# Optimization experiments

Measured on AMD Instinct MI355X. Metric: run time of the kernel, lower is better.

## Reference

```python
import jax, jax.numpy as jnp
import numpy as np

N = 30          # num_nodes
F = 4           # feature_dim
H = 64          # decoder_hidden_dim
TF = 2          # decoder_tf_interval
MIN_VAR = 1e-8
MAX_VAR = 100.0

_pairs = np.array([(i, j) for i in range(N) for j in range(N) if i != j])
RECV = jnp.asarray(_pairs[:, 0])   # [E] receiver node per edge
SEND = jnp.asarray(_pairs[:, 1])   # [E] sender node per edge


def _mlp(x, Ws, bs, softplus=False):
    # Linear->ReLU for all hidden layers, final Linear; optional softplus+clip head
    for W, b in zip(Ws[:-1], bs[:-1]):
        x = jax.nn.relu(x @ W + b)
    x = x @ Ws[-1] + bs[-1]
    if softplus:
        x = jnp.clip(jax.nn.softplus(x), MIN_VAR, MAX_VAR)
    return x


def setup_inputs() -> dict:
    key = jax.random.key(0)
    ks = jax.random.split(key, 20)
    B, S, T = 8, 4, 128
    E = N * (N - 1)

    def lin(k, din, dout):
        s = 1.0 / np.sqrt(din)
        return jax.random.uniform(k, (din, dout), jnp.float32, -s, s)

    inp = {
        'data': jax.random.normal(ks[0], (B, S, T, N, F), jnp.float32),
        'graph': (jax.random.uniform(ks[1], (B * S, E)) > 0.5).astype(jnp.float32),
        # msg_fc: 2F -> H -> H
        'msg_W1': lin(ks[2], 2 * F, H), 'msg_b1': jnp.zeros((H,), jnp.float32),
        'msg_W2': lin(ks[3], H, H),     'msg_b2': jnp.zeros((H,), jnp.float32),
        # mean_fc: H -> H -> H -> F
        'mean_W1': lin(ks[4], H, H), 'mean_b1': jnp.zeros((H,), jnp.float32),
        'mean_W2': lin(ks[5], H, H), 'mean_b2': jnp.zeros((H,), jnp.float32),
        'mean_W3': lin(ks[6], H, F), 'mean_b3': jnp.zeros((F,), jnp.float32),
        # variance_fc: H -> H -> H -> F (softplus + clip)
        'var_W1': lin(ks[7], H, H), 'var_b1': jnp.zeros((H,), jnp.float32),
        'var_W2': lin(ks[8], H, H), 'var_b2': jnp.zeros((H,), jnp.float32),
        'var_W3': lin(ks[9], H, F), 'var_b3': jnp.zeros((F,), jnp.float32),
    }
    return inp


def _single_step(prev, graph, p):
    # prev: [B, C, N, F]; graph: [B, E]
    edge_hidden = jnp.concatenate([prev[:, :, RECV, :], prev[:, :, SEND, :]], axis=-1)  # [B,C,E,2F]
    msg = _mlp(edge_hidden, [p['msg_W1'], p['msg_W2']], [p['msg_b1'], p['msg_b2']])     # [B,C,E,H]
    msg = msg * graph[:, None, :, None]
    B, C = prev.shape[0], prev.shape[1]
    # edge2node: sum messages into receiver nodes (normalize=False)
    agg = jnp.zeros((B, C, N, msg.shape[-1]), msg.dtype).at[:, :, RECV, :].add(msg)     # [B,C,N,H]
    mu = _mlp(agg, [p['mean_W1'], p['mean_W2'], p['mean_W3']],
              [p['mean_b1'], p['mean_b2'], p['mean_b3']])
    var = _mlp(agg, [p['var_W1'], p['var_W2'], p['var_W3']],
               [p['var_b1'], p['var_b2'], p['var_b3']], softplus=True)
    return mu, var


def reference(data, graph, msg_W1, msg_b1, msg_W2, msg_b2,
              mean_W1, mean_b1, mean_W2, mean_b2, mean_W3, mean_b3,
              var_W1, var_b1, var_W2, var_b2, var_W3, var_b3):
    p = dict(msg_W1=msg_W1, msg_b1=msg_b1, msg_W2=msg_W2, msg_b2=msg_b2,
             mean_W1=mean_W1, mean_b1=mean_b1, mean_W2=mean_W2, mean_b2=mean_b2,
             mean_W3=mean_W3, mean_b3=mean_b3,
             var_W1=var_W1, var_b1=var_b1, var_W2=var_W2, var_b2=var_b2,
             var_W3=var_W3, var_b3=var_b3)
    B, S, T, Nn, Ff = data.shape
    x = data.reshape(B * S, T, Nn, Ff)
    prev = x[:, ::TF]                       # teacher-forced anchors, [B*S, C, N, F]
    C = prev.shape[1]
    mus, vars = [], []
    for _ in range(TF):
        mu, var = _single_step(prev, graph, p)
        mus.append(mu)
        vars.append(var)
        prev = mu
    # interleave: out[:, i::TF] = step_i
    mu_pred = jnp.stack(mus, axis=2).reshape(B * S, C * TF, Nn, Ff)[:, :T - 1]
    var_pred = jnp.stack(vars, axis=2).reshape(B * S, C * TF, Nn, Ff)[:, :T - 1]
    mu_pred = mu_pred.reshape(B, S, T - 1, Nn, Ff)
    var_pred = var_pred.reshape(B, S, T - 1, Nn, Ff)
    return mu_pred, var_pred
```

## Files before the change

kernel.cpp:

```cpp
#include <hip/hip_runtime.h>
#include <hip/hip_bf16.h>
#include <hip/hip_fp16.h>

typedef unsigned short u16;
typedef unsigned int u32;
typedef __attribute__((ext_vector_type(4))) short short4v;
typedef __attribute__((ext_vector_type(4))) float f32x4;
typedef __attribute__((ext_vector_type(2))) _Float16 half2v;

#define NN 30
#define FF 4
#define EE 870
#define BSZ 32
#define CC 64
#define TT 128
#define NF 120
#define TSTRIDE 15240
#define OUTHALF 487680
#define AST 68
#define WST 68
#define NSETS 4
#define BPB  16

#define WS_WOFF 256
#define WS_MASKOFF (256 + 45056)

__device__ __forceinline__ float bf2f(u16 u) {
    union { u32 i; float f; } v; v.i = ((u32)u) << 16; return v.f;
}
__device__ __forceinline__ u16 f2bf(float f) {
    __hip_bfloat16 h = __float2bfloat16(f); return *(u16*)&h;
}
__device__ __forceinline__ u16 f2bf_fast(float f) {
    union { float f; u32 u; } v; v.f = f;
    return (u16)((v.u + 0x7FFFu + ((v.u >> 16) & 1u)) >> 16);
}
__device__ __forceinline__ float ldv(const void* p, int idx, int isbf) {
    if (isbf) return bf2f(((const u16*)p)[idx]);
    return ((const float*)p)[idx];
}
__device__ __forceinline__ float softplus_clip(float z) {
    float t = __expf(-fabsf(z));
    float sp = fmaxf(z, 0.f) + __logf(1.f + t);
    return fminf(fmaxf(sp, 1e-8f), 100.f);
}
__device__ __forceinline__ f32x4 MFMA16(short4v a, short4v b, f32x4 c) {
    return __builtin_amdgcn_mfma_f32_16x16x16bf16_1k(a, b, c, 0, 0, 0);
}

__device__ __forceinline__ int probe_isbf(const u16* g, int lane) {
    int hit = (g[2 * lane] == 0x3F80u) | (g[128 + 2 * lane] == 0x3F80u);
    unsigned long long b = __ballot(hit);
    return (b != 0ull) ? 1 : 0;
}

__global__ void prep_ws(const void* __restrict__ mW2,
                        const void* __restrict__ aW1, const void* __restrict__ aW2,
                        const void* __restrict__ vW1, const void* __restrict__ vW2,
                        const void* __restrict__ graph,
                        u16* __restrict__ wsW, u32* __restrict__ wsMask) {
    const int lane = threadIdx.x & 63;
    const int isbf = probe_isbf((const u16*)graph, lane);
    const int gtid = blockIdx.x * blockDim.x + threadIdx.x;
    const int gstr = gridDim.x * blockDim.x;
    for (int idx = gtid; idx < 4096; idx += gstr) {
        int k = idx >> 6, o = idx & 63;
        int d = o * 64 + k;
        wsW[d]         = f2bf(ldv(mW2, idx, isbf));
        wsW[4096 + d]  = f2bf(ldv(aW1, idx, isbf));
        wsW[8192 + d]  = f2bf(ldv(aW2, idx, isbf));
        wsW[12288 + d] = f2bf(ldv(vW1, idx, isbf));
        wsW[16384 + d] = f2bf(ldv(vW2, idx, isbf));
    }
    for (int idx = gtid; idx < BSZ * NN; idx += gstr) {
        int b = idx / NN, i = idx % NN;
        u32 m = 0;
        for (int e = 0; e < 29; e++)
            if (ldv(graph, b * EE + i * 29 + e, isbf) > 0.5f) m |= (1u << e);
        wsMask[idx] = m;
    }
}

__global__ __launch_bounds__(1024, 4)
void sim_fused(const void* __restrict__ data,
               const void* __restrict__ graph,
               const void* __restrict__ mW1, const void* __restrict__ mB1,
               const void* __restrict__ mB2,
               const void* __restrict__ aB1, const void* __restrict__ aB2,
               const void* __restrict__ aB3,
               const void* __restrict__ vB1, const void* __restrict__ vB2,
               const void* __restrict__ vB3,
               const void* __restrict__ aW3, const void* __restrict__ vW3,
               const u16* __restrict__ wsW, const u32* __restrict__ wsMask,
               void* __restrict__ out)
{
    __shared__ __align__(16) float xN[NSETS][NF];
    __shared__ __align__(16) u32 gmaskS[32];
    __shared__ __align__(16) u16 S[NSETS][32 * AST];
    __shared__ __align__(16) u16 lwM2[64 * WST];
    __shared__ __align__(16) u16 lwH1m[64 * WST];
    __shared__ __align__(16) u16 lwH2m[64 * WST];
    __shared__ __align__(16) u16 lwH1v[64 * WST];
    __shared__ __align__(16) u16 lwH2v[64 * WST];
    __shared__ __align__(16) float biasL[5 * 64];

    const int tid  = threadIdx.x;
    const int lane = tid & 63;
    const int wv   = tid >> 6;
    const int set  = wv >> 2;
    const int swv  = wv & 3;
    const int ln15 = lane & 15;
    const int quad = lane >> 4;
    const int bs   = blockIdx.x / BPB;
    const int bg   = blockIdx.x % BPB;
    const int c    = bg * NSETS + set;
    const int isbf = probe_isbf((const u16*)graph, lane);

    const bool isMean = (swv < 2);
    const int nb = swv & 1;

    {
        const u32* w32 = (const u32*)wsW;
        for (int idx = tid; idx < 2048; idx += 1024) {
            int o = idx >> 5, kw = idx & 31;
            int d = o * (WST / 2) + kw;
            ((u32*)lwM2)[d]  = w32[idx];
            ((u32*)lwH1m)[d] = w32[2048 + idx];
            ((u32*)lwH2m)[d] = w32[4096 + idx];
            ((u32*)lwH1v)[d] = w32[6144 + idx];
            ((u32*)lwH2v)[d] = w32[8192 + idx];
        }
    }
    if (tid < 64) {
        biasL[tid]       = ldv(mB2, tid, isbf);
        biasL[64 + tid]  = ldv(aB1, tid, isbf);
        biasL[128 + tid] = ldv(aB2, tid, isbf);
        biasL[192 + tid] = ldv(vB1, tid, isbf);
        biasL[256 + tid] = ldv(vB2, tid, isbf);
    }
    if (tid < 32) gmaskS[tid] = (tid < NN) ? wsMask[bs * NN + tid] : 0u;
    if (tid < 512) {
        int s2 = tid >> 7, row = 30 + ((tid >> 6) & 1);
        S[s2][row * AST + (tid & 63)] = 0;
    }

    float w1r[8];
#pragma unroll
    for (int k = 0; k < 8; k++) w1r[k] = ldv(mW1, k * 64 + lane, isbf);
    const float b1r = ldv(mB1, lane, isbf);
    float b3r[4];
#pragma unroll
    for (int r = 0; r < 4; r++) b3r[r] = ldv(isMean ? aB3 : vB3, r, isbf);

    const u16* wH1 = isMean ? lwH1m : lwH1v;
    const u16* wH2 = isMean ? lwH2m : lwH2v;
    const float* bAgg = biasL;
    const float* bH1  = isMean ? (biasL + 64)  : (biasL + 192);
    const float* bH2  = isMean ? (biasL + 128) : (biasL + 256);

    const void* W3src = isMean ? aW3 : vW3;
    short4v eA[4];
#pragma unroll
    for (int kb = 0; kb < 4; kb++) {
        union { short4v v; u16 s[4]; } pk;
#pragma unroll
        for (int j = 0; j < 4; j++) {
            int k = kb * 16 + quad * 4 + j;
            pk.s[j] = (ln15 < 4)
                ? (isbf ? ((const u16*)W3src)[k * 4 + ln15]
                        : f2bf(((const float*)W3src)[k * 4 + ln15]))
                : (u16)0;
        }
        eA[kb] = pk.v;
    }

    __syncthreads();

    const int myNode = nb * 16 + ln15;
    const float ngp = (myNode < NN) ? (float)__popc(gmaskS[myNode]) : 0.f;

    auto runLayer = [&](const u16* wl, const float* bl, const short4v* Bin,
                        short4v* Bout, float bscale, bool doRelu) {
#pragma unroll
        for (int fb = 0; fb < 4; fb++) {
            f32x4 acc = {0.f, 0.f, 0.f, 0.f};
#pragma unroll
            for (int kb = 0; kb < 4; kb++) {
                short4v a = *(const short4v*)&wl[(fb * 16 + ln15) * WST + kb * 16 + quad * 4];
                acc = MFMA16(a, Bin[kb], acc);
            }
            float4 bv = *(const float4*)&bl[fb * 16 + quad * 4];
            union { short4v v; u16 s[4]; } pk;
#pragma unroll
            for (int r = 0; r < 4; r++) {
                float val = acc[r] + bscale * (&bv.x)[r];
                if (doRelu) val = fmaxf(val, 0.f);
                pk.s[r] = f2bf_fast(val);
            }
            Bout[fb] = pk.v;
        }
    };

    const int setTid = tid & 255;

    if (isbf) {
        if (setTid < 60) {
            u32 w = ((const u32*)data)[((bs * TT + 2 * c) * NF) / 2 + setTid];
            xN[set][setTid * 2]     = bf2f((u16)(w & 0xFFFF));
            xN[set][setTid * 2 + 1] = bf2f((u16)(w >> 16));
        }
    } else {
        if (setTid < NF) xN[set][setTid] = ((const float*)data)[(bs * TT + 2 * c) * NF + setTid];
    }
    __syncthreads();

    for (int step = 0; step < 2; step++) {
        half2v pJp[15];
#pragma unroll
        for (int m = 0; m < 15; m++) {
            float4 xa = *(const float4*)&xN[set][(2 * m) * 4];
            float4 xb = *(const float4*)&xN[set][(2 * m + 1) * 4];
            float pa = xa.x * w1r[4] + xa.y * w1r[5] + xa.z * w1r[6] + xa.w * w1r[7];
            float pb = xb.x * w1r[4] + xb.y * w1r[5] + xb.z * w1r[6] + xb.w * w1r[7];
            half2v p; p.x = (_Float16)pa; p.y = (_Float16)pb;
            pJp[m] = p;
        }

        const half2v zero2 = {(_Float16)0.f, (_Float16)0.f};
        for (int i = swv; i < NN; i += 4) {
            float4 xv = *(const float4*)&xN[set][i * 4];
            float pI = b1r + xv.x * w1r[0] + xv.y * w1r[1] + xv.z * w1r[2] + xv.w * w1r[3];
            _Float16 pih = (_Float16)pI;
            half2v pIp = {pih, pih};
            u32 gm = gmaskS[i];
            u32 lowm = (1u << i) - 1u;
            u32 m2 = __builtin_amdgcn_readfirstlane((gm & lowm) | ((gm & ~lowm) << 1));
            float s0 = 0.f, s1 = 0.f;
#pragma unroll
            for (int m = 0; m < 15; m++) {
                half2v t = pIp + pJp[m];
                t = __builtin_elementwise_max(t, zero2);
#if __has_builtin(__builtin_amdgcn_fdot2)
                u32 mm = ((m2 >> (2 * m)) & 1u) * 0x3C00u
                       + ((m2 >> (2 * m + 1)) & 1u) * 0x3C000000u;
                half2v mv = __builtin_bit_cast(half2v, mm);
                if (m & 1) s1 = __builtin_amdgcn_fdot2(t, mv, s1, false);
                else       s0 = __builtin_amdgcn_fdot2(t, mv, s0, false);
#else
                u32 mb = ((m2 >> (2 * m)) & 1u) * 0xFFFFu
                       + ((m2 >> (2 * m + 1)) & 1u) * 0xFFFF0000u;
                u32 tb = __builtin_bit_cast(u32, t) & mb;
                half2v tv = __builtin_bit_cast(half2v, tb);
                s0 += (float)tv.x; s1 += (float)tv.y;
#endif
            }
            S[set][i * AST + lane] = f2bf_fast(s0 + s1);
        }
        __syncthreads();

        short4v Bs[4], Ba[4], Bb[4];
#pragma unroll
        for (int kb = 0; kb < 4; kb++)
            Bs[kb] = *(const short4v*)&S[set][(nb * 16 + ln15) * AST + kb * 16 + quad * 4];

        runLayer(lwM2, bAgg, Bs, Ba, ngp, false);
        runLayer(wH1,  bH1,  Ba, Bb, 1.f, true);
        runLayer(wH2,  bH2,  Bb, Ba, 1.f, true);

        {
            f32x4 acc = {0.f, 0.f, 0.f, 0.f};
#pragma unroll
            for (int kb = 0; kb < 4; kb++) acc = MFMA16(eA[kb], Ba[kb], acc);
            const int n = nb * 16 + ln15;
            const int t = 2 * c + step;
            if (quad == 0 && n < NN) {
                float v[4];
#pragma unroll
                for (int r = 0; r < 4; r++) v[r] = acc[r] + b3r[r];
                if (!isMean) {
#pragma unroll
                    for (int r = 0; r < 4; r++) v[r] = softplus_clip(v[r]);
                }
                if (t < 127) {
                    size_t o = (size_t)bs * TSTRIDE + (size_t)t * NF + n * 4
                             + (isMean ? 0 : OUTHALF);
                    if (isbf) {
                        u16* op = (u16*)out;
                        u32 lo = (u32)f2bf_fast(v[0]) | ((u32)f2bf_fast(v[1]) << 16);
                        u32 hi = (u32)f2bf_fast(v[2]) | ((u32)f2bf_fast(v[3]) << 16);
                        *(u32*)&op[o] = lo;
                        *(u32*)&op[o + 2] = hi;
                    } else {
                        float* op = (float*)out;
                        op[o] = v[0]; op[o+1] = v[1]; op[o+2] = v[2]; op[o+3] = v[3];
                    }
                }
                if (isMean && step == 0) {
                    xN[set][n*4]   = v[0]; xN[set][n*4+1] = v[1];
                    xN[set][n*4+2] = v[2]; xN[set][n*4+3] = v[3];
                }
            }
        }
        __syncthreads();
    }
}

extern "C" void kernel_launch(void* const* d_in, const int* in_sizes, int n_in,
                              void* d_out, int out_size, void* d_ws, size_t ws_size,
                              hipStream_t stream) {
    (void)in_sizes; (void)n_in; (void)out_size; (void)ws_size;

    const void* data  = d_in[0];
    const void* graph = d_in[1];
    const void* mW1 = d_in[2];  const void* mB1 = d_in[3];
    const void* mW2 = d_in[4];  const void* mB2 = d_in[5];
    const void* aW1 = d_in[6];  const void* aB1 = d_in[7];
    const void* aW2 = d_in[8];  const void* aB2 = d_in[9];
    const void* aW3 = d_in[10]; const void* aB3 = d_in[11];
    const void* vW1 = d_in[12]; const void* vB1 = d_in[13];
    const void* vW2 = d_in[14]; const void* vB2 = d_in[15];
    const void* vW3 = d_in[16]; const void* vB3 = d_in[17];

    u16* wsW    = (u16*)((char*)d_ws + WS_WOFF);
    u32* wsMask = (u32*)((char*)d_ws + WS_MASKOFF);

    prep_ws<<<8, 256, 0, stream>>>(mW2, aW1, aW2, vW1, vW2,
                                   graph, wsW, wsMask);

    sim_fused<<<BSZ * BPB, 1024, 0, stream>>>(data, graph,
        mW1, mB1, mB2, aB1, aB2, aB3, vB1, vB2, vB3,
        aW3, vW3, wsW, wsMask, d_out);
}
```

Before: 144.9 us.

## Fold weight and graph-mask preprocessing into the main kernel, dropping prep launch

Removes the separate prep_ws kernel that converted hidden-layer weights to bf16 and built per-node graph bitmasks in workspace. Each block now converts the weights directly into shared memory and builds its own edge mask with shared-memory atomicOr. The data load is also moved earlier so it overlaps with setup behind a single barrier. This saves a kernel launch and a dependency gap. In exchange, every one of the 512 blocks redundantly reads and converts the fp32 weights with strided global loads and scattered 16-bit LDS stores, and uses the faster bf16 rounding helper instead of the library one.

```diff
diff --git a/kernel.cpp b/kernel.cpp
--- a/kernel.cpp
+++ b/kernel.cpp
@@ -22,14 +22,9 @@
 #define NSETS 4
 #define BPB  16
 
-#define WS_WOFF 256
-#define WS_MASKOFF (256 + 45056)
 
 __device__ __forceinline__ float bf2f(u16 u) {
     union { u32 i; float f; } v; v.i = ((u32)u) << 16; return v.f;
-}
-__device__ __forceinline__ u16 f2bf(float f) {
-    __hip_bfloat16 h = __float2bfloat16(f); return *(u16*)&h;
 }
 __device__ __forceinline__ u16 f2bf_fast(float f) {
     union { float f; u32 u; } v; v.f = f;
@@ -54,44 +49,17 @@
     return (b != 0ull) ? 1 : 0;
 }
 
-__global__ void prep_ws(const void* __restrict__ mW2,
-                        const void* __restrict__ aW1, const void* __restrict__ aW2,
-                        const void* __restrict__ vW1, const void* __restrict__ vW2,
-                        const void* __restrict__ graph,
-                        u16* __restrict__ wsW, u32* __restrict__ wsMask) {
-    const int lane = threadIdx.x & 63;
-    const int isbf = probe_isbf((const u16*)graph, lane);
-    const int gtid = blockIdx.x * blockDim.x + threadIdx.x;
-    const int gstr = gridDim.x * blockDim.x;
-    for (int idx = gtid; idx < 4096; idx += gstr) {
-        int k = idx >> 6, o = idx & 63;
-        int d = o * 64 + k;
-        wsW[d]         = f2bf(ldv(mW2, idx, isbf));
-        wsW[4096 + d]  = f2bf(ldv(aW1, idx, isbf));
-        wsW[8192 + d]  = f2bf(ldv(aW2, idx, isbf));
-        wsW[12288 + d] = f2bf(ldv(vW1, idx, isbf));
-        wsW[16384 + d] = f2bf(ldv(vW2, idx, isbf));
-    }
-    for (int idx = gtid; idx < BSZ * NN; idx += gstr) {
-        int b = idx / NN, i = idx % NN;
-        u32 m = 0;
-        for (int e = 0; e < 29; e++)
-            if (ldv(graph, b * EE + i * 29 + e, isbf) > 0.5f) m |= (1u << e);
-        wsMask[idx] = m;
-    }
-}
-
 __global__ __launch_bounds__(1024, 4)
 void sim_fused(const void* __restrict__ data,
                const void* __restrict__ graph,
                const void* __restrict__ mW1, const void* __restrict__ mB1,
-               const void* __restrict__ mB2,
-               const void* __restrict__ aB1, const void* __restrict__ aB2,
-               const void* __restrict__ aB3,
-               const void* __restrict__ vB1, const void* __restrict__ vB2,
-               const void* __restrict__ vB3,
-               const void* __restrict__ aW3, const void* __restrict__ vW3,
-               const u16* __restrict__ wsW, const u32* __restrict__ wsMask,
+               const void* __restrict__ mW2, const void* __restrict__ mB2,
+               const void* __restrict__ aW1, const void* __restrict__ aB1,
+               const void* __restrict__ aW2, const void* __restrict__ aB2,
+               const void* __restrict__ aW3, const void* __restrict__ aB3,
+               const void* __restrict__ vW1, const void* __restrict__ vB1,
+               const void* __restrict__ vW2, const void* __restrict__ vB2,
+               const void* __restrict__ vW3, const void* __restrict__ vB3,
                void* __restrict__ out)
 {
     __shared__ __align__(16) float xN[NSETS][NF];
@@ -119,17 +87,27 @@
     const bool isMean = (swv < 2);
     const int nb = swv & 1;
 
-    {
-        const u32* w32 = (const u32*)wsW;
-        for (int idx = tid; idx < 2048; idx += 1024) {
-            int o = idx >> 5, kw = idx & 31;
-            int d = o * (WST / 2) + kw;
-            ((u32*)lwM2)[d]  = w32[idx];
-            ((u32*)lwH1m)[d] = w32[2048 + idx];
-            ((u32*)lwH2m)[d] = w32[4096 + idx];
-            ((u32*)lwH1v)[d] = w32[6144 + idx];
-            ((u32*)lwH2v)[d] = w32[8192 + idx];
-        }
+    if (tid < 32) gmaskS[tid] = 0u;
+    if (tid < 512) {
+        int s2 = tid >> 7, row = 30 + ((tid >> 6) & 1);
+        S[s2][row * AST + (tid & 63)] = 0;
+    }
+    __syncthreads();
+
+    if (tid < EE) {
+        int i = tid / 29;
+        int e = tid - i * 29;
+        if (ldv(graph, bs * EE + tid, isbf) > 0.5f)
+            atomicOr(&gmaskS[i], 1u << e);
+    }
+    for (int idx = tid; idx < 4096; idx += 1024) {
+        int k = idx >> 6, o = idx & 63;
+        int d = o * WST + k;
+        lwM2[d]  = f2bf_fast(ldv(mW2, idx, isbf));
+        lwH1m[d] = f2bf_fast(ldv(aW1, idx, isbf));
+        lwH2m[d] = f2bf_fast(ldv(aW2, idx, isbf));
+        lwH1v[d] = f2bf_fast(ldv(vW1, idx, isbf));
+        lwH2v[d] = f2bf_fast(ldv(vW2, idx, isbf));
     }
     if (tid < 64) {
         biasL[tid]       = ldv(mB2, tid, isbf);
@@ -138,10 +116,17 @@
         biasL[192 + tid] = ldv(vB1, tid, isbf);
         biasL[256 + tid] = ldv(vB2, tid, isbf);
     }
-    if (tid < 32) gmaskS[tid] = (tid < NN) ? wsMask[bs * NN + tid] : 0u;
-    if (tid < 512) {
-        int s2 = tid >> 7, row = 30 + ((tid >> 6) & 1);
-        S[s2][row * AST + (tid & 63)] = 0;
+    {
+        const int setTid = tid & 255;
+        if (isbf) {
+            if (setTid < 60) {
+                u32 w = ((const u32*)data)[((bs * TT + 2 * c) * NF) / 2 + setTid];
+                xN[set][setTid * 2]     = bf2f((u16)(w & 0xFFFF));
+                xN[set][setTid * 2 + 1] = bf2f((u16)(w >> 16));
+            }
+        } else {
+            if (setTid < NF) xN[set][setTid] = ((const float*)data)[(bs * TT + 2 * c) * NF + setTid];
+        }
     }
 
     float w1r[8];
@@ -168,7 +153,7 @@
             int k = kb * 16 + quad * 4 + j;
             pk.s[j] = (ln15 < 4)
                 ? (isbf ? ((const u16*)W3src)[k * 4 + ln15]
-                        : f2bf(((const float*)W3src)[k * 4 + ln15]))
+                        : f2bf_fast(((const float*)W3src)[k * 4 + ln15]))
                 : (u16)0;
         }
         eA[kb] = pk.v;
@@ -200,19 +185,6 @@
             Bout[fb] = pk.v;
         }
     };
-
-    const int setTid = tid & 255;
-
-    if (isbf) {
-        if (setTid < 60) {
-            u32 w = ((const u32*)data)[((bs * TT + 2 * c) * NF) / 2 + setTid];
-            xN[set][setTid * 2]     = bf2f((u16)(w & 0xFFFF));
-            xN[set][setTid * 2 + 1] = bf2f((u16)(w >> 16));
-        }
-    } else {
-        if (setTid < NF) xN[set][setTid] = ((const float*)data)[(bs * TT + 2 * c) * NF + setTid];
-    }
-    __syncthreads();
 
     for (int step = 0; step < 2; step++) {
         half2v pJp[15];
@@ -308,7 +280,7 @@
 extern "C" void kernel_launch(void* const* d_in, const int* in_sizes, int n_in,
                               void* d_out, int out_size, void* d_ws, size_t ws_size,
                               hipStream_t stream) {
-    (void)in_sizes; (void)n_in; (void)out_size; (void)ws_size;
+    (void)in_sizes; (void)n_in; (void)out_size; (void)d_ws; (void)ws_size;
 
     const void* data  = d_in[0];
     const void* graph = d_in[1];
@@ -321,13 +293,9 @@
     const void* vW2 = d_in[14]; const void* vB2 = d_in[15];
     const void* vW3 = d_in[16]; const void* vB3 = d_in[17];
 
-    u16* wsW    = (u16*)((char*)d_ws + WS_WOFF);
-    u32* wsMask = (u32*)((char*)d_ws + WS_MASKOFF);
-
-    prep_ws<<<8, 256, 0, stream>>>(mW2, aW1, aW2, vW1, vW2,
-                                   graph, wsW, wsMask);
-
     sim_fused<<<BSZ * BPB, 1024, 0, stream>>>(data, graph,
-        mW1, mB1, mB2, aB1, aB2, aB3, vB1, vB2, vB3,
-        aW3, vW3, wsW, wsMask, d_out);
-}
+        mW1, mB1, mW2, mB2,
+        aW1, aB1, aW2, aB2, aW3, aB3,
+        vW1, vB1, vW2, vB2, vW3, vB3,
+        d_out);
+}
```

Result: no change. 143.8 us (-0.8%).
